# Kernel optimization log

Measured on AMD Instinct MI355X. Metric: run time of the kernel, lower is better.

## Reference

```python
import jax, jax.numpy as jnp
import numpy as np

N, M, B, L, D = 100000, 256, 8, 128, 64
COORD_MAX = 1024


def setup_inputs() -> dict:
    key = jax.random.key(0)
    ks = jax.random.split(key, 9)
    # batch ids sorted so the original loop's centroid_offset == column index
    clu_b = jnp.sort(jax.random.randint(ks[0], (N, 1), 0, B))
    cen_b = jnp.sort(jax.random.randint(ks[1], (M, 1), 0, B))
    clu_xyz = jax.random.randint(ks[2], (N, 3), 0, COORD_MAX)
    cen_xyz = jax.random.randint(ks[3], (M, 3), 0, COORD_MAX)
    return {
        "cluster_coords": jnp.concatenate([clu_b, clu_xyz], axis=1).astype(jnp.int32),
        "centroid_coords": jnp.concatenate([cen_b, cen_xyz], axis=1).astype(jnp.int32),
        "cluster_feats": jax.random.normal(ks[4], (N, L), jnp.float32),
        "centroid_feats": jax.random.normal(ks[5], (M, L), jnp.float32),
        "centroid_conf": jax.random.uniform(ks[6], (M, 1), jnp.float32),
        "W": jax.random.normal(ks[7], (L, D), jnp.float32) * 0.05,
        "b": jax.random.normal(ks[8], (D,), jnp.float32) * 0.05,
    }


def reference(cluster_coords, centroid_coords, cluster_feats, centroid_feats,
              centroid_conf, W, b):
    # pointwise Conv3d(k=1) == linear on features
    clu = cluster_feats @ W + b                      # [N, D]
    nrm = jnp.maximum(jnp.linalg.norm(clu, axis=1, keepdims=True), 1e-12)
    clu = clu / nrm                                  # F.normalize(p=2, dim=1)
    cen = centroid_conf * (centroid_feats @ W + b)   # [M, D]

    # same-batch mask replaces the python loop + scatter
    valid = cluster_coords[:, 0][:, None] == centroid_coords[:, 0][None, :]  # [N, M]

    # pairwise L2 distance on spatial coords via squared expansion (exact for small ints)
    cc = cluster_coords[:, 1:].astype(jnp.float32)   # [N, 3]
    ec = centroid_coords[:, 1:].astype(jnp.float32)  # [M, 3]
    d2 = (jnp.sum(cc * cc, axis=1)[:, None]
          + jnp.sum(ec * ec, axis=1)[None, :]
          - 2.0 * cc @ ec.T)
    dist = jnp.maximum(jnp.sqrt(jnp.maximum(d2, 0.0)), 0.1)  # clamp(min=0.1)

    logits = jnp.where(valid, -dist, -jnp.inf)
    attn = jax.nn.softmax(logits, axis=-1)           # per-row over same-batch centroids
    attn = jnp.where(valid, attn, 0.0)               # rows w/ no centroids -> 0 (matches zeros init)

    out = (clu @ cen.T) * attn                       # [N, M]
    return out
```

## Files before the change

kernel.cpp:

```cpp
#include <hip/hip_runtime.h>
#include <stdint.h>


#define NN 100000
#define MM 256
#define LL 128
#define DD 64
#define NTILES (NN / 16)

typedef float f32x4 __attribute__((ext_vector_type(4)));
typedef __bf16 bf16x8 __attribute__((ext_vector_type(8)));

union U16x8 { uint4 u; bf16x8 v; unsigned short s[8]; };
union BU { __bf16 b; unsigned short u; };

static __device__ __forceinline__ unsigned short f2bf(float f) {
  union { float f; unsigned int i; } t; t.f = f;
  unsigned int x = t.i;
  x += 0x7fffu + ((x >> 16) & 1u);
  return (unsigned short)(x >> 16);
}

__global__ __launch_bounds__(256) void prep_kernel(
    const int* __restrict__ cen_coords,
    const float* __restrict__ cen_feats,
    const float* __restrict__ conf,
    const float* __restrict__ W,
    const float* __restrict__ bvec,
    unsigned short* __restrict__ cen_ws,
    unsigned short* __restrict__ wt_ws,
    float4* __restrict__ cmeta_ws)
{
  int tid = threadIdx.x;
  if (blockIdx.x < 16) {
    int m = blockIdx.x * 16 + (tid >> 4);
    int c = tid & 15;
    float a0 = 0.f, a1 = 0.f, a2 = 0.f, a3 = 0.f;
    for (int l = 0; l < LL; l++) {
      float f = cen_feats[m * LL + l];
      const float* wr = W + l * DD + c;
      a0 += f * wr[0];  a1 += f * wr[16];
      a2 += f * wr[32]; a3 += f * wr[48];
    }
    float cf = conf[m];
    cen_ws[m * DD + c +  0] = f2bf(cf * (a0 + bvec[c +  0]));
    cen_ws[m * DD + c + 16] = f2bf(cf * (a1 + bvec[c + 16]));
    cen_ws[m * DD + c + 32] = f2bf(cf * (a2 + bvec[c + 32]));
    cen_ws[m * DD + c + 48] = f2bf(cf * (a3 + bvec[c + 48]));
  } else {
    for (int i = tid; i < LL * DD; i += 256) {
      int l = i >> 6, d = i & 63;
      wt_ws[d * LL + l] = f2bf(W[l * DD + d]);
    }
    {
      int4 cc = ((const int4*)cen_coords)[tid];
      float4 f; f.x = (float)cc.x; f.y = (float)cc.y; f.z = (float)cc.z; f.w = (float)cc.w;
      cmeta_ws[tid] = f;
    }
  }
}

__global__ __launch_bounds__(256) void main_kernel(
    const int4* __restrict__ clu_coords4,
    const float* __restrict__ feats,
    const float* __restrict__ bvec,
    const unsigned short* __restrict__ cen_ws,
    const unsigned short* __restrict__ wt_ws,
    const float4* __restrict__ cmeta,
    float* __restrict__ out)
{
  __shared__ __align__(16) unsigned short clu_s[4][16 * 72];

  int tid = threadIdx.x;
  int wave = tid >> 6, lane = tid & 63;
  int q = lane >> 4, c = lane & 15;
  int tile = blockIdx.x * 4 + wave;
  bool live = tile < NTILES;

  float inv_nrm[4], scale[4];
  float dv[16][4];
  if (live) {
    int rb[4]; float rx[4], ry[4], rz[4];
#pragma unroll
    for (int r = 0; r < 4; r++) {
      int4 rm = clu_coords4[tile * 16 + q * 4 + r];
      rb[r] = rm.x; rx[r] = (float)rm.y; ry[r] = (float)rm.z; rz[r] = (float)rm.w;
    }

    const f32x4* fb = (const f32x4*)(feats + (size_t)(tile * 16 + c) * LL);
    f32x4 f[8];
#pragma unroll
    for (int ks = 0; ks < 4; ks++) {
      f[ks * 2 + 0] = __builtin_nontemporal_load(&fb[ks * 8 + q * 2]);
      f[ks * 2 + 1] = __builtin_nontemporal_load(&fb[ks * 8 + q * 2 + 1]);
    }

    float dmin[4] = {1e30f, 1e30f, 1e30f, 1e30f};
#pragma unroll
    for (int mt = 0; mt < 16; mt++) {
      float4 cm = cmeta[mt * 16 + c];
      int cbatch = (int)cm.x;
#pragma unroll
      for (int r = 0; r < 4; r++) {
        float dx = rx[r] - cm.y, dy = ry[r] - cm.z, dz = rz[r] - cm.w;
        float d = fmaxf(sqrtf(dx*dx + dy*dy + dz*dz), 0.1f);
        d = (cbatch == rb[r]) ? d : 1e30f;
        dv[mt][r] = d;
        dmin[r] = fminf(dmin[r], d);
      }
    }

    f32x4 acc[4] = {{0,0,0,0},{0,0,0,0},{0,0,0,0},{0,0,0,0}};
    const uint4* wb = (const uint4*)wt_ws;
#pragma unroll
    for (int ks = 0; ks < 4; ks++) {
      f32x4 f0 = f[ks * 2], f1 = f[ks * 2 + 1];
      U16x8 a;
      a.v = (bf16x8){(__bf16)f0[0], (__bf16)f0[1], (__bf16)f0[2], (__bf16)f0[3],
                     (__bf16)f1[0], (__bf16)f1[1], (__bf16)f1[2], (__bf16)f1[3]};
#pragma unroll
      for (int nt = 0; nt < 4; nt++) {
        U16x8 b; b.u = wb[(nt * 16 + c) * 16 + ks * 4 + q];
        acc[nt] = __builtin_amdgcn_mfma_f32_16x16x32_bf16(a.v, b.v, acc[nt], 0, 0, 0);
      }
    }
#pragma unroll
    for (int nt = 0; nt < 4; nt++) {
      float bv = bvec[nt * 16 + c];
      acc[nt][0] += bv; acc[nt][1] += bv; acc[nt][2] += bv; acc[nt][3] += bv;
    }
#pragma unroll
    for (int r = 0; r < 4; r++) {
      float s = acc[0][r]*acc[0][r] + acc[1][r]*acc[1][r] + acc[2][r]*acc[2][r] + acc[3][r]*acc[3][r];
      s += __shfl_xor(s, 1); s += __shfl_xor(s, 2); s += __shfl_xor(s, 4); s += __shfl_xor(s, 8);
      inv_nrm[r] = 1.0f / fmaxf(sqrtf(s), 1e-12f);
    }
#pragma unroll
    for (int nt = 0; nt < 4; nt++)
#pragma unroll
      for (int r = 0; r < 4; r++) {
        BU t; t.b = (__bf16)acc[nt][r];
        clu_s[wave][(q * 4 + r) * 72 + nt * 16 + c] = t.u;
      }

#pragma unroll
    for (int r = 0; r < 4; r++) {
      dmin[r] = fminf(dmin[r], __shfl_xor(dmin[r], 1));
      dmin[r] = fminf(dmin[r], __shfl_xor(dmin[r], 2));
      dmin[r] = fminf(dmin[r], __shfl_xor(dmin[r], 4));
      dmin[r] = fminf(dmin[r], __shfl_xor(dmin[r], 8));
      dmin[r] = fminf(dmin[r], 1e29f);
    }
    float rsum[4] = {0.f, 0.f, 0.f, 0.f};
#pragma unroll
    for (int mt = 0; mt < 16; mt++)
#pragma unroll
      for (int r = 0; r < 4; r++) {
        float e = __expf(dmin[r] - dv[mt][r]);
        dv[mt][r] = e;
        rsum[r] += e;
      }
#pragma unroll
    for (int r = 0; r < 4; r++) {
      rsum[r] += __shfl_xor(rsum[r], 1);
      rsum[r] += __shfl_xor(rsum[r], 2);
      rsum[r] += __shfl_xor(rsum[r], 4);
      rsum[r] += __shfl_xor(rsum[r], 8);
      scale[r] = (rsum[r] > 0.f) ? inv_nrm[r] / rsum[r] : 0.f;
    }
  }
  __syncthreads();
  if (!live) return;

  const uint4* cb = (const uint4*)(clu_s[wave]);
  U16x8 a0, a1;
  a0.u = cb[c * 9 + q];
  a1.u = cb[c * 9 + 4 + q];

  const uint4* cenb = (const uint4*)cen_ws;
  size_t orow = (size_t)(tile * 16) * MM;
  float* op0 = out + orow + (size_t)(q * 4 + 0) * MM;
  float* op1 = op0 + MM, *op2 = op1 + MM, *op3 = op2 + MM;
#pragma unroll
  for (int mt = 0; mt < 16; mt++) {
    U16x8 b0, b1;
    b0.u = cenb[(mt * 16 + c) * 8 + q];
    b1.u = cenb[(mt * 16 + c) * 8 + 4 + q];
    f32x4 dacc = {0, 0, 0, 0};
    dacc = __builtin_amdgcn_mfma_f32_16x16x32_bf16(a0.v, b0.v, dacc, 0, 0, 0);
    dacc = __builtin_amdgcn_mfma_f32_16x16x32_bf16(a1.v, b1.v, dacc, 0, 0, 0);
    int m = mt * 16 + c;
    __builtin_nontemporal_store(dacc[0] * dv[mt][0] * scale[0], op0 + m);
    __builtin_nontemporal_store(dacc[1] * dv[mt][1] * scale[1], op1 + m);
    __builtin_nontemporal_store(dacc[2] * dv[mt][2] * scale[2], op2 + m);
    __builtin_nontemporal_store(dacc[3] * dv[mt][3] * scale[3], op3 + m);
  }
}

extern "C" void kernel_launch(void* const* d_in, const int* in_sizes, int n_in,
                              void* d_out, int out_size, void* d_ws, size_t ws_size,
                              hipStream_t stream) {
  const int* clu_coords = (const int*)d_in[0];
  const int* cen_coords = (const int*)d_in[1];
  const float* clu_feats = (const float*)d_in[2];
  const float* cen_feats = (const float*)d_in[3];
  const float* conf      = (const float*)d_in[4];
  const float* W         = (const float*)d_in[5];
  const float* bvec      = (const float*)d_in[6];
  float* out = (float*)d_out;

  char* ws = (char*)d_ws;
  unsigned short* cen_ws = (unsigned short*)ws;
  unsigned short* wt_ws  = (unsigned short*)(ws + 32768);
  float4* cmeta_ws       = (float4*)(ws + 32768 + 16384);

  prep_kernel<<<17, 256, 0, stream>>>(cen_coords, cen_feats, conf, W, bvec,
                                      cen_ws, wt_ws, cmeta_ws);
  main_kernel<<<(NTILES + 3) / 4, 256, 0, stream>>>(
      (const int4*)clu_coords, clu_feats, bvec, cen_ws, wt_ws, cmeta_ws, out);
}
```

Baseline: 213.9 us.

## Split cluster projection GEMM into separate kernel staging bf16 fragments in workspace

Splits the fused main kernel in two. The first kernel projects the cluster features, normalizes them, and writes the bf16 MFMA A-fragments to a workspace buffer. The second kernel computes distances, softmax and the output GEMM from those fragments. The split is meant to lower register pressure and raise occupancy in each kernel, at the cost of an extra launch and a round trip of about 12.8 MB through memory. Output stores also change from nontemporal to regular stores.

```diff
diff --git a/kernel.cpp b/kernel.cpp
--- a/kernel.cpp
+++ b/kernel.cpp
@@ -9,9 +9,10 @@
 #define NTILES (NN / 16)
 
 typedef float f32x4 __attribute__((ext_vector_type(4)));
+typedef unsigned int u32x4 __attribute__((ext_vector_type(4)));
 typedef __bf16 bf16x8 __attribute__((ext_vector_type(8)));
 
-union U16x8 { uint4 u; bf16x8 v; unsigned short s[8]; };
+union U16x8 { uint4 u; u32x4 e; bf16x8 v; unsigned short s[8]; };
 union BU { __bf16 b; unsigned short u; };
 
 static __device__ __forceinline__ unsigned short f2bf(float f) {
@@ -60,14 +61,11 @@
   }
 }
 
-__global__ __launch_bounds__(256) void main_kernel(
-    const int4* __restrict__ clu_coords4,
+__global__ __launch_bounds__(256) void gemm1_kernel(
     const float* __restrict__ feats,
     const float* __restrict__ bvec,
-    const unsigned short* __restrict__ cen_ws,
     const unsigned short* __restrict__ wt_ws,
-    const float4* __restrict__ cmeta,
-    float* __restrict__ out)
+    u32x4* __restrict__ clu_ws)
 {
   __shared__ __align__(16) unsigned short clu_s[4][16 * 72];
 
@@ -77,44 +75,14 @@
   int tile = blockIdx.x * 4 + wave;
   bool live = tile < NTILES;
 
-  float inv_nrm[4], scale[4];
-  float dv[16][4];
   if (live) {
-    int rb[4]; float rx[4], ry[4], rz[4];
-#pragma unroll
-    for (int r = 0; r < 4; r++) {
-      int4 rm = clu_coords4[tile * 16 + q * 4 + r];
-      rb[r] = rm.x; rx[r] = (float)rm.y; ry[r] = (float)rm.z; rz[r] = (float)rm.w;
-    }
-
     const f32x4* fb = (const f32x4*)(feats + (size_t)(tile * 16 + c) * LL);
-    f32x4 f[8];
-#pragma unroll
-    for (int ks = 0; ks < 4; ks++) {
-      f[ks * 2 + 0] = __builtin_nontemporal_load(&fb[ks * 8 + q * 2]);
-      f[ks * 2 + 1] = __builtin_nontemporal_load(&fb[ks * 8 + q * 2 + 1]);
-    }
-
-    float dmin[4] = {1e30f, 1e30f, 1e30f, 1e30f};
-#pragma unroll
-    for (int mt = 0; mt < 16; mt++) {
-      float4 cm = cmeta[mt * 16 + c];
-      int cbatch = (int)cm.x;
-#pragma unroll
-      for (int r = 0; r < 4; r++) {
-        float dx = rx[r] - cm.y, dy = ry[r] - cm.z, dz = rz[r] - cm.w;
-        float d = fmaxf(sqrtf(dx*dx + dy*dy + dz*dz), 0.1f);
-        d = (cbatch == rb[r]) ? d : 1e30f;
-        dv[mt][r] = d;
-        dmin[r] = fminf(dmin[r], d);
-      }
-    }
-
     f32x4 acc[4] = {{0,0,0,0},{0,0,0,0},{0,0,0,0},{0,0,0,0}};
     const uint4* wb = (const uint4*)wt_ws;
 #pragma unroll
     for (int ks = 0; ks < 4; ks++) {
-      f32x4 f0 = f[ks * 2], f1 = f[ks * 2 + 1];
+      f32x4 f0 = __builtin_nontemporal_load(&fb[ks * 8 + q * 2]);
+      f32x4 f1 = __builtin_nontemporal_load(&fb[ks * 8 + q * 2 + 1]);
       U16x8 a;
       a.v = (bf16x8){(__bf16)f0[0], (__bf16)f0[1], (__bf16)f0[2], (__bf16)f0[3],
                      (__bf16)f1[0], (__bf16)f1[1], (__bf16)f1[2], (__bf16)f1[3]};
@@ -133,7 +101,8 @@
     for (int r = 0; r < 4; r++) {
       float s = acc[0][r]*acc[0][r] + acc[1][r]*acc[1][r] + acc[2][r]*acc[2][r] + acc[3][r]*acc[3][r];
       s += __shfl_xor(s, 1); s += __shfl_xor(s, 2); s += __shfl_xor(s, 4); s += __shfl_xor(s, 8);
-      inv_nrm[r] = 1.0f / fmaxf(sqrtf(s), 1e-12f);
+      float invn = 1.0f / fmaxf(sqrtf(s), 1e-12f);
+      acc[0][r] *= invn; acc[1][r] *= invn; acc[2][r] *= invn; acc[3][r] *= invn;
     }
 #pragma unroll
     for (int nt = 0; nt < 4; nt++)
@@ -142,40 +111,81 @@
         BU t; t.b = (__bf16)acc[nt][r];
         clu_s[wave][(q * 4 + r) * 72 + nt * 16 + c] = t.u;
       }
-
-#pragma unroll
-    for (int r = 0; r < 4; r++) {
-      dmin[r] = fminf(dmin[r], __shfl_xor(dmin[r], 1));
-      dmin[r] = fminf(dmin[r], __shfl_xor(dmin[r], 2));
-      dmin[r] = fminf(dmin[r], __shfl_xor(dmin[r], 4));
-      dmin[r] = fminf(dmin[r], __shfl_xor(dmin[r], 8));
-      dmin[r] = fminf(dmin[r], 1e29f);
-    }
-    float rsum[4] = {0.f, 0.f, 0.f, 0.f};
-#pragma unroll
-    for (int mt = 0; mt < 16; mt++)
-#pragma unroll
-      for (int r = 0; r < 4; r++) {
-        float e = __expf(dmin[r] - dv[mt][r]);
-        dv[mt][r] = e;
-        rsum[r] += e;
-      }
-#pragma unroll
-    for (int r = 0; r < 4; r++) {
-      rsum[r] += __shfl_xor(rsum[r], 1);
-      rsum[r] += __shfl_xor(rsum[r], 2);
-      rsum[r] += __shfl_xor(rsum[r], 4);
-      rsum[r] += __shfl_xor(rsum[r], 8);
-      scale[r] = (rsum[r] > 0.f) ? inv_nrm[r] / rsum[r] : 0.f;
-    }
   }
   __syncthreads();
   if (!live) return;
-
-  const uint4* cb = (const uint4*)(clu_s[wave]);
+  const u32x4* cb = (const u32x4*)(clu_s[wave]);
+  u32x4 a0 = cb[c * 9 + q];
+  u32x4 a1 = cb[c * 9 + 4 + q];
+  clu_ws[(size_t)tile * 128 + lane] = a0;
+  clu_ws[(size_t)tile * 128 + 64 + lane] = a1;
+}
+
+__global__ __launch_bounds__(256) void main_kernel(
+    const int4* __restrict__ clu_coords4,
+    const u32x4* __restrict__ clu_ws,
+    const unsigned short* __restrict__ cen_ws,
+    const float4* __restrict__ cmeta,
+    float* __restrict__ out)
+{
+  int tid = threadIdx.x;
+  int wave = tid >> 6, lane = tid & 63;
+  int q = lane >> 4, c = lane & 15;
+  int tile = blockIdx.x * 4 + wave;
+  if (tile >= NTILES) return;
+
   U16x8 a0, a1;
-  a0.u = cb[c * 9 + q];
-  a1.u = cb[c * 9 + 4 + q];
+  a0.e = __builtin_nontemporal_load(&clu_ws[(size_t)tile * 128 + lane]);
+  a1.e = __builtin_nontemporal_load(&clu_ws[(size_t)tile * 128 + 64 + lane]);
+
+  int rb[4]; float rx[4], ry[4], rz[4];
+#pragma unroll
+  for (int r = 0; r < 4; r++) {
+    int4 rm = clu_coords4[tile * 16 + q * 4 + r];
+    rb[r] = rm.x; rx[r] = (float)rm.y; ry[r] = (float)rm.z; rz[r] = (float)rm.w;
+  }
+
+  float dv[16][4];
+  float dmin[4] = {1e30f, 1e30f, 1e30f, 1e30f};
+#pragma unroll
+  for (int mt = 0; mt < 16; mt++) {
+    float4 cm = cmeta[mt * 16 + c];
+    int cbatch = (int)cm.x;
+#pragma unroll
+    for (int r = 0; r < 4; r++) {
+      float dx = rx[r] - cm.y, dy = ry[r] - cm.z, dz = rz[r] - cm.w;
+      float d = fmaxf(sqrtf(dx*dx + dy*dy + dz*dz), 0.1f);
+      d = (cbatch == rb[r]) ? d : 1e30f;
+      dv[mt][r] = d;
+      dmin[r] = fminf(dmin[r], d);
+    }
+  }
+#pragma unroll
+  for (int r = 0; r < 4; r++) {
+    dmin[r] = fminf(dmin[r], __shfl_xor(dmin[r], 1));
+    dmin[r] = fminf(dmin[r], __shfl_xor(dmin[r], 2));
+    dmin[r] = fminf(dmin[r], __shfl_xor(dmin[r], 4));
+    dmin[r] = fminf(dmin[r], __shfl_xor(dmin[r], 8));
+    dmin[r] = fminf(dmin[r], 1e29f);
+  }
+  float rsum[4] = {0.f, 0.f, 0.f, 0.f};
+#pragma unroll
+  for (int mt = 0; mt < 16; mt++)
+#pragma unroll
+    for (int r = 0; r < 4; r++) {
+      float e = __expf(dmin[r] - dv[mt][r]);
+      dv[mt][r] = e;
+      rsum[r] += e;
+    }
+  float scale[4];
+#pragma unroll
+  for (int r = 0; r < 4; r++) {
+    rsum[r] += __shfl_xor(rsum[r], 1);
+    rsum[r] += __shfl_xor(rsum[r], 2);
+    rsum[r] += __shfl_xor(rsum[r], 4);
+    rsum[r] += __shfl_xor(rsum[r], 8);
+    scale[r] = (rsum[r] > 0.f) ? 1.f / rsum[r] : 0.f;
+  }
 
   const uint4* cenb = (const uint4*)cen_ws;
   size_t orow = (size_t)(tile * 16) * MM;
@@ -190,10 +200,10 @@
     dacc = __builtin_amdgcn_mfma_f32_16x16x32_bf16(a0.v, b0.v, dacc, 0, 0, 0);
     dacc = __builtin_amdgcn_mfma_f32_16x16x32_bf16(a1.v, b1.v, dacc, 0, 0, 0);
     int m = mt * 16 + c;
-    __builtin_nontemporal_store(dacc[0] * dv[mt][0] * scale[0], op0 + m);
-    __builtin_nontemporal_store(dacc[1] * dv[mt][1] * scale[1], op1 + m);
-    __builtin_nontemporal_store(dacc[2] * dv[mt][2] * scale[2], op2 + m);
-    __builtin_nontemporal_store(dacc[3] * dv[mt][3] * scale[3], op3 + m);
+    op0[m] = dacc[0] * dv[mt][0] * scale[0];
+    op1[m] = dacc[1] * dv[mt][1] * scale[1];
+    op2[m] = dacc[2] * dv[mt][2] * scale[2];
+    op3[m] = dacc[3] * dv[mt][3] * scale[3];
   }
 }
 
@@ -213,9 +223,12 @@
   unsigned short* cen_ws = (unsigned short*)ws;
   unsigned short* wt_ws  = (unsigned short*)(ws + 32768);
   float4* cmeta_ws       = (float4*)(ws + 32768 + 16384);
+  u32x4* clu_ws          = (u32x4*)(ws + 65536);
 
   prep_kernel<<<17, 256, 0, stream>>>(cen_coords, cen_feats, conf, W, bvec,
                                       cen_ws, wt_ws, cmeta_ws);
+  gemm1_kernel<<<(NTILES + 3) / 4, 256, 0, stream>>>(
+      clu_feats, bvec, wt_ws, clu_ws);
   main_kernel<<<(NTILES + 3) / 4, 256, 0, stream>>>(
-      (const int4*)clu_coords, clu_feats, bvec, cen_ws, wt_ws, cmeta_ws, out);
-}
+      (const int4*)clu_coords, clu_ws, cen_ws, cmeta_ws, out);
+}
```

After: 204.4 us. -4.4%, faster.
